# Optimization experiments

Hardware: AMD Instinct MI355X
Metric: run time of the kernel (lower is better)

Reference implementation:

```python
import jax, jax.numpy as jnp
import numpy as np

HEADS = 8
DIM_HEAD = 64


def setup_inputs() -> dict:
    key = jax.random.key(0)
    k1, k2, k3 = jax.random.split(key, 3)
    B, F, N_PATCH, DIM = 8, 16, 196, 512
    seq = 1 + F * N_PATCH  # 3137
    inner = HEADS * DIM_HEAD  # 512
    x = jax.random.normal(k1, (B, seq, DIM), dtype=jnp.float32)
    Wqkv = jax.random.normal(k2, (DIM, 3 * inner), dtype=jnp.float32) * (DIM ** -0.5)
    Wout = jax.random.normal(k3, (inner, DIM), dtype=jnp.float32) * (inner ** -0.5)
    bout = jnp.zeros((DIM,), dtype=jnp.float32)
    return {"x": x, "Wqkv": Wqkv, "Wout": Wout, "bout": bout, "f": F}


def _attn(q, k, v):
    # q: [b, i, d], k/v: [b, j, d]
    sim = jnp.einsum('bid,bjd->bij', q, k)
    a = jax.nn.softmax(sim, axis=-1)
    return jnp.einsum('bij,bjd->bid', a, v)


def reference(x, Wqkv, Wout, bout, f):
    B, N, D = x.shape
    h, dh = HEADS, DIM_HEAD
    scale = dh ** -0.5
    qkv = x @ Wqkv  # [B, N, 3*h*dh]
    q, k, v = jnp.split(qkv, 3, axis=-1)

    def to_bh(t):  # 'b n (h d) -> (b h) n d'
        return t.reshape(B, N, h, dh).transpose(0, 2, 1, 3).reshape(B * h, N, dh)

    q, k, v = to_bh(q), to_bh(k), to_bh(v)
    q = q * scale

    cls_q, q_ = q[:, :1], q[:, 1:]
    cls_k, k_ = k[:, :1], k[:, 1:]
    cls_v, v_ = v[:, :1], v[:, 1:]

    # cls token attends to all tokens
    cls_out = _attn(cls_q, k, v)  # [(b h), 1, dh]

    n = (N - 1) // f
    # 'b (f n) d -> (b f) n d'
    def split_frames(t):
        return t.reshape(B * h, f, n, dh).reshape(B * h * f, n, dh)

    q_, k_, v_ = split_frames(q_), split_frames(k_), split_frames(v_)

    # 'b () d -> (b r) () d' with r = f
    cls_k = jnp.repeat(cls_k, f, axis=0)
    cls_v = jnp.repeat(cls_v, f, axis=0)
    k_ = jnp.concatenate((cls_k, k_), axis=1)  # [(b h f), n+1, dh]
    v_ = jnp.concatenate((cls_v, v_), axis=1)

    out = _attn(q_, k_, v_)  # [(b h f), n, dh]
    out = out.reshape(B * h, f * n, dh)  # '(b f) n d -> b (f n) d'
    out = jnp.concatenate((cls_out, out), axis=1)  # [(b h), N, dh]
    # '(b h) n d -> b n (h d)'
    out = out.reshape(B, h, N, dh).transpose(0, 2, 1, 3).reshape(B, N, h * dh)
    return out @ Wout + bout
```

## Files before the change

### kernel.cpp

```cpp
#include <hip/hip_runtime.h>
#include <hip/hip_bf16.h>

#define B_    8
#define F_    16
#define NP_   196
#define SEQ_  3137
#define H_    8
#define DH_   64
#define BH_   64
#define M_    25096
#define MPAD_ 25216
#define DIM_  512
#define NQKV_ 1536

typedef _Float16 half8_t __attribute__((ext_vector_type(8)));
typedef _Float16 half4_t __attribute__((ext_vector_type(4)));
typedef float f32x4 __attribute__((ext_vector_type(4)));

#define XH_OFF     ((size_t)0)
#define WQKVT_OFF  ((size_t)25821184)
#define WOUTT_OFF  ((size_t)27394048)
#define QH_OFF     ((size_t)27918336)
#define KH_OFF     ((size_t)53616640)
#define VH_OFF     ((size_t)79314944)
#define ATTNH_OFF  ((size_t)105013248)
#define CLSP_OFF   XH_OFF

__device__ __forceinline__ void load_lds16(const _Float16* g, _Float16* l) {
  __builtin_amdgcn_global_load_lds(
      (const __attribute__((address_space(1))) void*)g,
      (__attribute__((address_space(3))) void*)l, 16, 0, 0);
}

__device__ __forceinline__ int xcd_swz(int orig, int nwg) {
  int q = nwg >> 3, r = nwg & 7;
  int x = orig & 7, j = orig >> 3;
  return (x < r ? x * (q + 1) : r * (q + 1) + (x - r) * q) + j;
}

__global__ __launch_bounds__(256) void convert_x_kernel(
    const float* __restrict__ x, _Float16* __restrict__ xh) {
  const size_t n8 = (size_t)M_ * DIM_ / 8;
  for (size_t i = (size_t)blockIdx.x * blockDim.x + threadIdx.x; i < n8;
       i += (size_t)gridDim.x * blockDim.x) {
    float4 a = ((const float4*)x)[2 * i];
    float4 b = ((const float4*)x)[2 * i + 1];
    half8_t h;
    h[0] = (_Float16)a.x; h[1] = (_Float16)a.y; h[2] = (_Float16)a.z; h[3] = (_Float16)a.w;
    h[4] = (_Float16)b.x; h[5] = (_Float16)b.y; h[6] = (_Float16)b.z; h[7] = (_Float16)b.w;
    ((half8_t*)xh)[i] = h;
  }
}

__global__ __launch_bounds__(256) void transpose_conv2_kernel(
    const float* __restrict__ wqkv, _Float16* __restrict__ wqkvT,
    const float* __restrict__ wout, _Float16* __restrict__ woutT) {
  __shared__ float tile[32][33];
  int by = blockIdx.y;
  const float* in; _Float16* out; int C;
  if (by < 48) { in = wqkv; out = wqkvT; C = NQKV_; }
  else         { in = wout; out = woutT; C = DIM_;  by -= 48; }
  const int r0 = blockIdx.x * 32, c0 = by * 32;
  const int lr = threadIdx.x >> 5, lc = threadIdx.x & 31;
#pragma unroll
  for (int p = 0; p < 4; ++p) {
    int r = p * 8 + lr;
    tile[r][lc] = in[(size_t)(r0 + r) * C + c0 + lc];
  }
  __syncthreads();
#pragma unroll
  for (int p = 0; p < 4; ++p) {
    int rr = p * 8 + lr;
    out[(size_t)(c0 + rr) * DIM_ + r0 + lc] = (_Float16)tile[lc][rr];
  }
}

__device__ __forceinline__ void gemm_mainloop_f16(
    const _Float16* __restrict__ A, const _Float16* __restrict__ Bt,
    int m0, int n0, _Float16* As, _Float16* Bs, f32x4 acc[4][4]) {
  const int tid = threadIdx.x;
  const int w = tid >> 6, lane = tid & 63;
  const int wr = w >> 1, wc = w & 1;
  const int lrow = lane & 15;
  const int g = lane >> 4;
  const int sw = lane & 7;

  const int srow = lane >> 3;
  const int scol = ((lane & 7) ^ srow) << 3;

  for (int k0 = 0; k0 < DIM_; k0 += 64) {
#pragma unroll
    for (int i = 0; i < 4; ++i) {
      int c = w * 4 + i;
      int r = c * 8 + srow;
      load_lds16(A + (size_t)(m0 + r) * DIM_ + k0 + scol, As + c * 512);
      load_lds16(Bt + (size_t)(n0 + r) * DIM_ + k0 + scol, Bs + c * 512);
    }
    __syncthreads();

#pragma unroll
    for (int kk = 0; kk < 2; ++kk) {
      const int kf = ((kk * 4 + g) ^ sw) << 3;
      half8_t a[4], b[4];
#pragma unroll
      for (int m = 0; m < 4; ++m)
        a[m] = *(const half8_t*)(As + (wr * 64 + m * 16 + lrow) * 64 + kf);
#pragma unroll
      for (int n = 0; n < 4; ++n)
        b[n] = *(const half8_t*)(Bs + (wc * 64 + n * 16 + lrow) * 64 + kf);
#pragma unroll
      for (int m = 0; m < 4; ++m)
#pragma unroll
        for (int n = 0; n < 4; ++n)
          acc[m][n] = __builtin_amdgcn_mfma_f32_16x16x32_f16(a[m], b[n], acc[m][n], 0, 0, 0);
    }
    __syncthreads();
  }
}

__global__ __launch_bounds__(256) void qkv_gemm_kernel(
    const _Float16* __restrict__ xh, const _Float16* __restrict__ wqkvT,
    _Float16* __restrict__ qh, _Float16* __restrict__ kh, _Float16* __restrict__ vh) {
  __shared__ _Float16 As[128 * 64];
  __shared__ _Float16 Bs[128 * 64];
  const int nwg = 197 * 12;
  const int lin = xcd_swz(blockIdx.x, nwg);
  const int mb = lin / 12, nb = lin - mb * 12;
  const int m0 = mb * 128, n0 = nb * 128;

  f32x4 acc[4][4];
#pragma unroll
  for (int m = 0; m < 4; ++m)
#pragma unroll
    for (int n = 0; n < 4; ++n) acc[m][n] = (f32x4)0.f;

  gemm_mainloop_f16(xh, wqkvT, m0, n0, As, Bs, acc);

  const int tid = threadIdx.x;
  const int w = tid >> 6, lane = tid & 63;
  const int wr = w >> 1, wc = w & 1;
  const int g = lane >> 4, lrow = lane & 15;

  _Float16* stg = (w < 2) ? (As + w * 4096) : (Bs + (w - 2) * 4096);
  const int gcb0 = n0 + wc * 64;
  const int which = gcb0 >> 9;
  const int h = (gcb0 >> 6) & 7;
  const float scale = (which == 0) ? 0.125f : 1.0f;
  _Float16* dst = (which == 0) ? qh : (which == 1) ? kh : vh;

#pragma unroll
  for (int m = 0; m < 4; ++m)
#pragma unroll
    for (int n = 0; n < 4; ++n)
#pragma unroll
      for (int j = 0; j < 4; ++j) {
        int row = m * 16 + g * 4 + j;
        int col = n * 16 + lrow;
        int slot = (col >> 3) ^ (row & 7);
        stg[row * 64 + slot * 8 + (col & 7)] = (_Float16)(acc[m][n][j] * scale);
      }
  asm volatile("s_waitcnt lgkmcnt(0)" ::: "memory");
  __builtin_amdgcn_sched_barrier(0);

  const int rl = lane >> 3, cs = lane & 7;
#pragma unroll
  for (int rr = 0; rr < 8; ++rr) {
    int row = rr * 8 + rl;
    int grow = m0 + wr * 64 + row;
    if (grow < M_) {
      int b = grow / SEQ_;
      int t = grow - b * SEQ_;
      half8_t v = *(const half8_t*)(stg + row * 64 + ((cs ^ (row & 7)) << 3));
      *(half8_t*)(dst + ((size_t)(b * H_ + h) * SEQ_ + t) * DH_ + cs * 8) = v;
    }
  }
}

__global__ __launch_bounds__(256) void out_gemm_kernel(
    const _Float16* __restrict__ attnh, const _Float16* __restrict__ woutT,
    const float* __restrict__ bias, float* __restrict__ out) {
  __shared__ _Float16 As[128 * 64];
  __shared__ _Float16 Bs[128 * 64];
  const int nwg = 197 * 4;
  const int lin = xcd_swz(blockIdx.x, nwg);
  const int mb = lin >> 2, nb = lin & 3;
  const int m0 = mb * 128, n0 = nb * 128;

  f32x4 acc[4][4];
#pragma unroll
  for (int m = 0; m < 4; ++m)
#pragma unroll
    for (int n = 0; n < 4; ++n) acc[m][n] = (f32x4)0.f;

  gemm_mainloop_f16(attnh, woutT, m0, n0, As, Bs, acc);

  const int tid = threadIdx.x;
  const int w = tid >> 6, lane = tid & 63;
  const int wr = w >> 1, wc = w & 1;
#pragma unroll
  for (int n = 0; n < 4; ++n) {
    const int gcol = n0 + wc * 64 + n * 16 + (lane & 15);
    const float bv = bias[gcol];
#pragma unroll
    for (int m = 0; m < 4; ++m)
#pragma unroll
      for (int j = 0; j < 4; ++j) {
        int grow = m0 + wr * 64 + m * 16 + (lane >> 4) * 4 + j;
        if (grow < M_) out[(size_t)grow * DIM_ + gcol] = acc[m][n][j] + bv;
      }
  }
}

__global__ __launch_bounds__(256) void attn_kernel(
    const _Float16* __restrict__ qh, const _Float16* __restrict__ kh,
    const _Float16* __restrict__ vh, _Float16* __restrict__ attnh,
    float* __restrict__ clsp) {
  __shared__ _Float16 SMEM[36864];
  const int bx = blockIdx.x;
  const int tid = threadIdx.x;

  const int bh = bx >> 4, fi = bx & 15;
  const int b = bh >> 3, h = bh & 7;
  const int w = tid >> 6, lane = tid & 63;
  const int g = lane >> 4, lc = lane & 15;
  _Float16* KL = SMEM;
  _Float16* VT = SMEM + 13312;
  _Float16* Pb = SMEM + 28160;
  _Float16* tmp = Pb;
  _Float16* Pw = Pb + w * (16 * 136);

  const size_t base = (size_t)bh * SEQ_ * DH_;

  half8_t qb0[4], qb1[4];
#pragma unroll
  for (int it = 0; it < 4; ++it) {
    int qq = min((w + it * 4) * 16 + lc, NP_ - 1);
    const _Float16* qp = qh + base + (size_t)(1 + fi * NP_ + qq) * DH_ + g * 8;
    qb0[it] = *(const half8_t*)(qp);
    qb1[it] = *(const half8_t*)(qp + 32);
  }

  for (int i = 0; i < 7; ++i) {
    int gran = i * 256 + tid;
    if (gran < 1664) {
      int row = gran >> 3, cg = gran & 7;
      int rowtok = (row == 0) ? 0 : fi * NP_ + min(row, NP_);
      load_lds16(kh + base + (size_t)rowtok * DH_ + ((cg ^ (row & 7)) << 3),
                 KL + (i * 256 + (tid & 192)) * 8);
    }
  }

#pragma unroll
  for (int half = 0; half < 2; ++half) {
    const int r0 = half * 104;
#pragma unroll
    for (int i = 0; i < 4; ++i) {
      int c = i * 256 + tid;
      if (c < 832) {
        int row = c >> 3, cg = c & 7;
        int gr = r0 + row;
        int rowtok = (gr == 0) ? 0 : fi * NP_ + min(gr, NP_);
        load_lds16(vh + base + (size_t)rowtok * DH_ + ((cg ^ (row & 7)) << 3),
                   tmp + (i * 256 + (tid & 192)) * 8);
      }
    }
    if (half == 1) {
      for (int idx = tid; idx < 64 * 35; idx += 256) {
        int d = idx / 35;
        VT[d * 232 + 197 + (idx - d * 35)] = (_Float16)0.f;
      }
    }
    __syncthreads();
#pragma unroll
    for (int i = 0; i < 4; ++i) {
      int item = i * 256 + tid;
      if (item < 832) {
        int cg = item / 104;
        int key = item - cg * 104;
        int gk = r0 + key;
        if (gk <= 196) {
          half8_t v = *(const half8_t*)(tmp + key * 64 + ((cg ^ (key & 7)) << 3));
#pragma unroll
          for (int u = 0; u < 8; ++u) VT[(cg * 8 + u) * 232 + gk] = v[u];
        }
      }
    }
    __syncthreads();
  }

  const f32x4 zero4 = (f32x4)0.f;

#pragma unroll
  for (int it = 0; it < 4; ++it) {
    const int qt = w + it * 4;
    if (qt < 13) {
      f32x4 st[13];
#pragma unroll
      for (int t = 0; t < 13; ++t) {
        int key = t * 16 + lc;
        const _Float16* kp = KL + key * 64;
        half8_t ka0 = *(const half8_t*)(kp + ((g ^ (key & 7)) << 3));
        half8_t ka1 = *(const half8_t*)(kp + (((4 + g) ^ (key & 7)) << 3));
        st[t] = __builtin_amdgcn_mfma_f32_16x16x32_f16(ka0, qb0[it], zero4, 0, 0, 0);
        st[t] = __builtin_amdgcn_mfma_f32_16x16x32_f16(ka1, qb1[it], st[t], 0, 0, 0);
      }

      float mx = -1e30f;
#pragma unroll
      for (int t = 0; t < 13; ++t)
#pragma unroll
        for (int j = 0; j < 4; ++j) {
          int key = t * 16 + g * 4 + j;
          if (key >= 197) st[t][j] = -1e30f;
          mx = fmaxf(mx, st[t][j]);
        }
      mx = fmaxf(mx, __shfl_xor(mx, 16));
      mx = fmaxf(mx, __shfl_xor(mx, 32));
      float l = 0.f;
#pragma unroll
      for (int t = 0; t < 13; ++t)
#pragma unroll
        for (int j = 0; j < 4; ++j) {
          float p = __expf(st[t][j] - mx);
          st[t][j] = p;
          l += p;
        }
      l += __shfl_xor(l, 16);
      l += __shfl_xor(l, 32);
      const float inv = 1.f / l;

      f32x4 o[4];
#pragma unroll
      for (int dt = 0; dt < 4; ++dt) o[dt] = zero4;

#pragma unroll
      for (int t = 0; t < 8; ++t) {
        half4_t hp;
#pragma unroll
        for (int j = 0; j < 4; ++j) hp[j] = (_Float16)(st[t][j] * inv);
        *(half4_t*)(Pw + lc * 136 + t * 16 + g * 4) = hp;
      }
#pragma unroll
      for (int c = 0; c < 4; ++c) {
        half8_t pa = *(const half8_t*)(Pw + lc * 136 + c * 32 + g * 8);
#pragma unroll
        for (int dt = 0; dt < 4; ++dt) {
          half8_t vb = *(const half8_t*)(VT + (dt * 16 + lc) * 232 + c * 32 + g * 8);
          o[dt] = __builtin_amdgcn_mfma_f32_16x16x32_f16(pa, vb, o[dt], 0, 0, 0);
        }
      }

#pragma unroll
      for (int t = 8; t < 13; ++t) {
        half4_t hp;
#pragma unroll
        for (int j = 0; j < 4; ++j) hp[j] = (_Float16)(st[t][j] * inv);
        *(half4_t*)(Pw + lc * 104 + (t - 8) * 16 + g * 4) = hp;
      }
      {
        half4_t hz;
#pragma unroll
        for (int j = 0; j < 4; ++j) hz[j] = (_Float16)0.f;
        *(half4_t*)(Pw + lc * 104 + 80 + g * 4) = hz;
      }
#pragma unroll
      for (int c = 4; c < 7; ++c) {
        half8_t pa = *(const half8_t*)(Pw + lc * 104 + (c - 4) * 32 + g * 8);
#pragma unroll
        for (int dt = 0; dt < 4; ++dt) {
          half8_t vb = *(const half8_t*)(VT + (dt * 16 + lc) * 232 + c * 32 + g * 8);
          o[dt] = __builtin_amdgcn_mfma_f32_16x16x32_f16(pa, vb, o[dt], 0, 0, 0);
        }
      }

#pragma unroll
      for (int dt = 0; dt < 4; ++dt)
#pragma unroll
        for (int j = 0; j < 4; ++j) {
          int q = qt * 16 + g * 4 + j;
          if (q < NP_) {
            int tok = 1 + fi * NP_ + q;
            attnh[((size_t)(b * SEQ_) + tok) * DIM_ + h * DH_ + dt * 16 + lc] =
                (_Float16)o[dt][j];
          }
        }
    }
  }

  __syncthreads();
  float* qs  = (float*)Pb;
  float* pp  = qs + 64;
  float* red = pp + 256;
  if (tid < 64) qs[tid] = (float)qh[base + tid];
  __syncthreads();

  const int kmin = (fi == 0) ? 0 : 1;
  float sc = -1e30f;
  if (tid >= kmin && tid < 197) {
    float s = 0.f;
#pragma unroll
    for (int i = 0; i < 8; ++i) {
      half8_t kk = *(const half8_t*)(KL + tid * 64 + ((i ^ (tid & 7)) << 3));
#pragma unroll
      for (int u = 0; u < 8; ++u) s += qs[8 * i + u] * (float)kk[u];
    }
    sc = s;
  }
  red[tid] = sc; __syncthreads();
  for (int st = 128; st > 0; st >>= 1) {
    if (tid < st) red[tid] = fmaxf(red[tid], red[tid + st]);
    __syncthreads();
  }
  const float cm = red[0]; __syncthreads();

  float cp = (tid >= kmin && tid < 197) ? __expf(sc - cm) : 0.f;
  pp[tid] = cp;
  red[tid] = cp; __syncthreads();
  for (int st = 128; st > 0; st >>= 1) {
    if (tid < st) red[tid] += red[tid + st];
    __syncthreads();
  }
  const float clsum = red[0]; __syncthreads();

  const int d = tid & 63;
  float a = 0.f;
#pragma unroll 4
  for (int u = 0; u < 64; ++u) {
    int k = w * 64 + u;
    if (k <= 196) a += pp[k] * (float)VT[d * 232 + k];
  }
  red[tid] = a; __syncthreads();
  if (tid < 64) {
    float asum = red[tid] + red[64 + tid] + red[128 + tid] + red[192 + tid];
    float* P = clsp + (size_t)(bh * 16 + fi) * 72;
    P[tid] = asum;
    if (tid == 0) { P[64] = cm; P[65] = clsum; }
  }
}

__global__ __launch_bounds__(64) void cls_combine_kernel(
    const float* __restrict__ clsp, _Float16* __restrict__ attnh) {
  const int bh = blockIdx.x;
  const int b = bh >> 3, h = bh & 7;
  const int d = threadIdx.x;
  const float* P = clsp + (size_t)bh * 16 * 72;

  float m = -1e30f;
#pragma unroll
  for (int c = 0; c < 16; ++c) m = fmaxf(m, P[c * 72 + 64]);
  float l = 0.f, o = 0.f;
#pragma unroll
  for (int c = 0; c < 16; ++c) {
    float wgt = __expf(P[c * 72 + 64] - m);
    l += P[c * 72 + 65] * wgt;
    o += P[c * 72 + d] * wgt;
  }
  attnh[(size_t)(b * SEQ_) * DIM_ + h * DH_ + d] = (_Float16)(o / l);
}

extern "C" void kernel_launch(void* const* d_in, const int* in_sizes, int n_in,
                              void* d_out, int out_size, void* d_ws, size_t ws_size,
                              hipStream_t stream) {
  (void)in_sizes; (void)n_in; (void)out_size; (void)ws_size;
  const float* x    = (const float*)d_in[0];
  const float* wqkv = (const float*)d_in[1];
  const float* wout = (const float*)d_in[2];
  const float* bout = (const float*)d_in[3];
  char* ws = (char*)d_ws;
  _Float16* xh    = (_Float16*)(ws + XH_OFF);
  _Float16* wqkvT = (_Float16*)(ws + WQKVT_OFF);
  _Float16* woutT = (_Float16*)(ws + WOUTT_OFF);
  _Float16* qh    = (_Float16*)(ws + QH_OFF);
  _Float16* kh    = (_Float16*)(ws + KH_OFF);
  _Float16* vh    = (_Float16*)(ws + VH_OFF);
  _Float16* attnh = (_Float16*)(ws + ATTNH_OFF);
  float*    clsp  = (float*)(ws + CLSP_OFF);
  float* out = (float*)d_out;

  convert_x_kernel<<<2048, 256, 0, stream>>>(x, xh);
  {
    dim3 g(16, 64);
    transpose_conv2_kernel<<<g, 256, 0, stream>>>(wqkv, wqkvT, wout, woutT);
  }

  qkv_gemm_kernel<<<197 * 12, 256, 0, stream>>>(xh, wqkvT, qh, kh, vh);

  attn_kernel<<<BH_ * F_, 256, 0, stream>>>(qh, kh, vh, attnh, clsp);
  cls_combine_kernel<<<BH_, 64, 0, stream>>>(clsp, attnh);

  out_gemm_kernel<<<197 * 4, 256, 0, stream>>>(attnh, woutT, bout, out);
}
```

Baseline: 166.4 us.

## Enlarge GEMM tiles to 256x128 and fuse weight/x conversion kernels

Both the QKV and output GEMMs now use 256x128 tiles, with each wave computing 128x64. Out-of-range A rows are clamped to the last valid row instead of relying on padding. The per-k-step loads of the B tile are shared across twice as many output rows, which raises arithmetic intensity but halves the number of workgroups (1188 and 396). That may leave the output GEMM with too few blocks to fill all CUs and raises register pressure. The x conversion and weight transpose kernels are merged into one launch to remove a launch gap.

Measured after the change: 210.9 us. 26.7% more time.

```diff
diff --git a/kernel.cpp b/kernel.cpp
--- a/kernel.cpp
+++ b/kernel.cpp
@@ -9,7 +9,6 @@
 #define DH_   64
 #define BH_   64
 #define M_    25096
-#define MPAD_ 25216
 #define DIM_  512
 #define NQKV_ 1536
 
@@ -38,11 +37,36 @@
   return (x < r ? x * (q + 1) : r * (q + 1) + (x - r) * q) + j;
 }
 
-__global__ __launch_bounds__(256) void convert_x_kernel(
-    const float* __restrict__ x, _Float16* __restrict__ xh) {
+__global__ __launch_bounds__(256) void prep_kernel(
+    const float* __restrict__ x, _Float16* __restrict__ xh,
+    const float* __restrict__ wqkv, _Float16* __restrict__ wqkvT,
+    const float* __restrict__ wout, _Float16* __restrict__ woutT) {
+  if (blockIdx.x < 1024) {
+    __shared__ float tile[32][33];
+    int id = blockIdx.x;
+    int xb = id & 15, by = id >> 4;
+    const float* in; _Float16* out; int C;
+    if (by < 48) { in = wqkv; out = wqkvT; C = NQKV_; }
+    else         { in = wout; out = woutT; C = DIM_;  by -= 48; }
+    const int r0 = xb * 32, c0 = by * 32;
+    const int lr = threadIdx.x >> 5, lc = threadIdx.x & 31;
+#pragma unroll
+    for (int p = 0; p < 4; ++p) {
+      int r = p * 8 + lr;
+      tile[r][lc] = in[(size_t)(r0 + r) * C + c0 + lc];
+    }
+    __syncthreads();
+#pragma unroll
+    for (int p = 0; p < 4; ++p) {
+      int rr = p * 8 + lr;
+      out[(size_t)(c0 + rr) * DIM_ + r0 + lc] = (_Float16)tile[lc][rr];
+    }
+    return;
+  }
+  const int id = blockIdx.x - 1024;
   const size_t n8 = (size_t)M_ * DIM_ / 8;
-  for (size_t i = (size_t)blockIdx.x * blockDim.x + threadIdx.x; i < n8;
-       i += (size_t)gridDim.x * blockDim.x) {
+  for (size_t i = (size_t)id * 256 + threadIdx.x; i < n8;
+       i += (size_t)2048 * 256) {
     float4 a = ((const float4*)x)[2 * i];
     float4 b = ((const float4*)x)[2 * i + 1];
     half8_t h;
@@ -52,67 +76,48 @@
   }
 }
 
-__global__ __launch_bounds__(256) void transpose_conv2_kernel(
-    const float* __restrict__ wqkv, _Float16* __restrict__ wqkvT,
-    const float* __restrict__ wout, _Float16* __restrict__ woutT) {
-  __shared__ float tile[32][33];
-  int by = blockIdx.y;
-  const float* in; _Float16* out; int C;
-  if (by < 48) { in = wqkv; out = wqkvT; C = NQKV_; }
-  else         { in = wout; out = woutT; C = DIM_;  by -= 48; }
-  const int r0 = blockIdx.x * 32, c0 = by * 32;
-  const int lr = threadIdx.x >> 5, lc = threadIdx.x & 31;
-#pragma unroll
-  for (int p = 0; p < 4; ++p) {
-    int r = p * 8 + lr;
-    tile[r][lc] = in[(size_t)(r0 + r) * C + c0 + lc];
-  }
-  __syncthreads();
-#pragma unroll
-  for (int p = 0; p < 4; ++p) {
-    int rr = p * 8 + lr;
-    out[(size_t)(c0 + rr) * DIM_ + r0 + lc] = (_Float16)tile[lc][rr];
-  }
-}
-
-__device__ __forceinline__ void gemm_mainloop_f16(
+__device__ __forceinline__ void gemm_mainloop_f16_w128(
     const _Float16* __restrict__ A, const _Float16* __restrict__ Bt,
-    int m0, int n0, _Float16* As, _Float16* Bs, f32x4 acc[4][4]) {
+    int m0, int n0, int maxA, _Float16* As, _Float16* Bs, f32x4 acc[8][4]) {
   const int tid = threadIdx.x;
   const int w = tid >> 6, lane = tid & 63;
-  const int wr = w >> 1, wc = w & 1;
+  const int wm = w >> 1, wn = w & 1;
   const int lrow = lane & 15;
   const int g = lane >> 4;
   const int sw = lane & 7;
 
-  const int srow = lane >> 3;
-  const int scol = ((lane & 7) ^ srow) << 3;
-
   for (int k0 = 0; k0 < DIM_; k0 += 64) {
 #pragma unroll
+    for (int i = 0; i < 8; ++i) {
+      int c = i * 256 + tid;
+      int row = c >> 3, s = c & 7;
+      int ra = min(m0 + row, maxA);
+      load_lds16(A + (size_t)ra * DIM_ + k0 + ((s ^ (row & 7)) << 3),
+                 As + (i * 256 + (tid & 192)) * 8);
+    }
+#pragma unroll
     for (int i = 0; i < 4; ++i) {
-      int c = w * 4 + i;
-      int r = c * 8 + srow;
-      load_lds16(A + (size_t)(m0 + r) * DIM_ + k0 + scol, As + c * 512);
-      load_lds16(Bt + (size_t)(n0 + r) * DIM_ + k0 + scol, Bs + c * 512);
+      int c = i * 256 + tid;
+      int row = c >> 3, s = c & 7;
+      load_lds16(Bt + (size_t)(n0 + row) * DIM_ + k0 + ((s ^ (row & 7)) << 3),
+                 Bs + (i * 256 + (tid & 192)) * 8);
     }
     __syncthreads();
 
 #pragma unroll
     for (int kk = 0; kk < 2; ++kk) {
       const int kf = ((kk * 4 + g) ^ sw) << 3;
-      half8_t a[4], b[4];
-#pragma unroll
-      for (int m = 0; m < 4; ++m)
-        a[m] = *(const half8_t*)(As + (wr * 64 + m * 16 + lrow) * 64 + kf);
+      half8_t b[4];
 #pragma unroll
       for (int n = 0; n < 4; ++n)
-        b[n] = *(const half8_t*)(Bs + (wc * 64 + n * 16 + lrow) * 64 + kf);
-#pragma unroll
-      for (int m = 0; m < 4; ++m)
+        b[n] = *(const half8_t*)(Bs + (wn * 64 + n * 16 + lrow) * 64 + kf);
+#pragma unroll
+      for (int m = 0; m < 8; ++m) {
+        half8_t a = *(const half8_t*)(As + (wm * 128 + m * 16 + lrow) * 64 + kf);
 #pragma unroll
         for (int n = 0; n < 4; ++n)
-          acc[m][n] = __builtin_amdgcn_mfma_f32_16x16x32_f16(a[m], b[n], acc[m][n], 0, 0, 0);
+          acc[m][n] = __builtin_amdgcn_mfma_f32_16x16x32_f16(a, b[n], acc[m][n], 0, 0, 0);
+      }
     }
     __syncthreads();
   }
@@ -121,57 +126,65 @@
 __global__ __launch_bounds__(256) void qkv_gemm_kernel(
     const _Float16* __restrict__ xh, const _Float16* __restrict__ wqkvT,
     _Float16* __restrict__ qh, _Float16* __restrict__ kh, _Float16* __restrict__ vh) {
-  __shared__ _Float16 As[128 * 64];
+  __shared__ _Float16 As[256 * 64];
   __shared__ _Float16 Bs[128 * 64];
-  const int nwg = 197 * 12;
+  const int nwg = 99 * 12;
   const int lin = xcd_swz(blockIdx.x, nwg);
   const int mb = lin / 12, nb = lin - mb * 12;
-  const int m0 = mb * 128, n0 = nb * 128;
-
-  f32x4 acc[4][4];
-#pragma unroll
-  for (int m = 0; m < 4; ++m)
+  const int m0 = mb * 256, n0 = nb * 128;
+
+  f32x4 acc[8][4];
+#pragma unroll
+  for (int m = 0; m < 8; ++m)
 #pragma unroll
     for (int n = 0; n < 4; ++n) acc[m][n] = (f32x4)0.f;
 
-  gemm_mainloop_f16(xh, wqkvT, m0, n0, As, Bs, acc);
+  gemm_mainloop_f16_w128(xh, wqkvT, m0, n0, M_ - 1, As, Bs, acc);
 
   const int tid = threadIdx.x;
   const int w = tid >> 6, lane = tid & 63;
-  const int wr = w >> 1, wc = w & 1;
+  const int wm = w >> 1, wn = w & 1;
   const int g = lane >> 4, lrow = lane & 15;
 
-  _Float16* stg = (w < 2) ? (As + w * 4096) : (Bs + (w - 2) * 4096);
-  const int gcb0 = n0 + wc * 64;
+  _Float16* stg = As + w * 4096;
+  const int gcb0 = n0 + wn * 64;
   const int which = gcb0 >> 9;
   const int h = (gcb0 >> 6) & 7;
   const float scale = (which == 0) ? 0.125f : 1.0f;
   _Float16* dst = (which == 0) ? qh : (which == 1) ? kh : vh;
-
-#pragma unroll
-  for (int m = 0; m < 4; ++m)
-#pragma unroll
-    for (int n = 0; n < 4; ++n)
-#pragma unroll
-      for (int j = 0; j < 4; ++j) {
-        int row = m * 16 + g * 4 + j;
-        int col = n * 16 + lrow;
-        int slot = (col >> 3) ^ (row & 7);
-        stg[row * 64 + slot * 8 + (col & 7)] = (_Float16)(acc[m][n][j] * scale);
-      }
-  asm volatile("s_waitcnt lgkmcnt(0)" ::: "memory");
-  __builtin_amdgcn_sched_barrier(0);
-
   const int rl = lane >> 3, cs = lane & 7;
-#pragma unroll
-  for (int rr = 0; rr < 8; ++rr) {
-    int row = rr * 8 + rl;
-    int grow = m0 + wr * 64 + row;
-    if (grow < M_) {
-      int b = grow / SEQ_;
-      int t = grow - b * SEQ_;
-      half8_t v = *(const half8_t*)(stg + row * 64 + ((cs ^ (row & 7)) << 3));
-      *(half8_t*)(dst + ((size_t)(b * H_ + h) * SEQ_ + t) * DH_ + cs * 8) = v;
+
+#pragma unroll
+  for (int r0 = 0; r0 < 2; ++r0) {
+#pragma unroll
+    for (int mm = 0; mm < 4; ++mm) {
+      int m = r0 * 4 + mm;
+#pragma unroll
+      for (int n = 0; n < 4; ++n)
+#pragma unroll
+        for (int j = 0; j < 4; ++j) {
+          int row2 = mm * 16 + g * 4 + j;
+          int col = n * 16 + lrow;
+          int slot = (col >> 3) ^ (row2 & 7);
+          stg[row2 * 64 + slot * 8 + (col & 7)] = (_Float16)(acc[m][n][j] * scale);
+        }
+    }
+    asm volatile("s_waitcnt lgkmcnt(0)" ::: "memory");
+    __builtin_amdgcn_sched_barrier(0);
+#pragma unroll
+    for (int rr = 0; rr < 8; ++rr) {
+      int row2 = rr * 8 + rl;
+      int grow = m0 + wm * 128 + r0 * 64 + row2;
+      if (grow < M_) {
+        int b = grow / SEQ_;
+        int t = grow - b * SEQ_;
+        half8_t v = *(const half8_t*)(stg + row2 * 64 + ((cs ^ (row2 & 7)) << 3));
+        *(half8_t*)(dst + ((size_t)(b * H_ + h) * SEQ_ + t) * DH_ + cs * 8) = v;
+      }
+    }
+    if (r0 == 0) {
+      asm volatile("s_waitcnt lgkmcnt(0)" ::: "memory");
+      __builtin_amdgcn_sched_barrier(0);
     }
   }
 }
@@ -179,33 +192,34 @@
 __global__ __launch_bounds__(256) void out_gemm_kernel(
     const _Float16* __restrict__ attnh, const _Float16* __restrict__ woutT,
     const float* __restrict__ bias, float* __restrict__ out) {
-  __shared__ _Float16 As[128 * 64];
+  __shared__ _Float16 As[256 * 64];
   __shared__ _Float16 Bs[128 * 64];
-  const int nwg = 197 * 4;
+  const int nwg = 99 * 4;
   const int lin = xcd_swz(blockIdx.x, nwg);
   const int mb = lin >> 2, nb = lin & 3;
-  const int m0 = mb * 128, n0 = nb * 128;
-
-  f32x4 acc[4][4];
-#pragma unroll
-  for (int m = 0; m < 4; ++m)
+  const int m0 = mb * 256, n0 = nb * 128;
+
+  f32x4 acc[8][4];
+#pragma unroll
+  for (int m = 0; m < 8; ++m)
 #pragma unroll
     for (int n = 0; n < 4; ++n) acc[m][n] = (f32x4)0.f;
 
-  gemm_mainloop_f16(attnh, woutT, m0, n0, As, Bs, acc);
+  gemm_mainloop_f16_w128(attnh, woutT, m0, n0, M_ - 1, As, Bs, acc);
 
   const int tid = threadIdx.x;
   const int w = tid >> 6, lane = tid & 63;
-  const int wr = w >> 1, wc = w & 1;
+  const int wm = w >> 1, wn = w & 1;
+  const int g = lane >> 4, lrow = lane & 15;
 #pragma unroll
   for (int n = 0; n < 4; ++n) {
-    const int gcol = n0 + wc * 64 + n * 16 + (lane & 15);
+    const int gcol = n0 + wn * 64 + n * 16 + lrow;
     const float bv = bias[gcol];
 #pragma unroll
-    for (int m = 0; m < 4; ++m)
+    for (int m = 0; m < 8; ++m)
 #pragma unroll
       for (int j = 0; j < 4; ++j) {
-        int grow = m0 + wr * 64 + m * 16 + (lane >> 4) * 4 + j;
+        int grow = m0 + wm * 128 + m * 16 + g * 4 + j;
         if (grow < M_) out[(size_t)grow * DIM_ + gcol] = acc[m][n][j] + bv;
       }
   }
@@ -477,16 +491,12 @@
   float*    clsp  = (float*)(ws + CLSP_OFF);
   float* out = (float*)d_out;
 
-  convert_x_kernel<<<2048, 256, 0, stream>>>(x, xh);
-  {
-    dim3 g(16, 64);
-    transpose_conv2_kernel<<<g, 256, 0, stream>>>(wqkv, wqkvT, wout, woutT);
-  }
-
-  qkv_gemm_kernel<<<197 * 12, 256, 0, stream>>>(xh, wqkvT, qh, kh, vh);
+  prep_kernel<<<3072, 256, 0, stream>>>(x, xh, wqkv, wqkvT, wout, woutT);
+
+  qkv_gemm_kernel<<<99 * 12, 256, 0, stream>>>(xh, wqkvT, qh, kh, vh);
 
   attn_kernel<<<BH_ * F_, 256, 0, stream>>>(qh, kh, vh, attnh, clsp);
   cls_combine_kernel<<<BH_, 64, 0, stream>>>(clsp, attnh);
 
-  out_gemm_kernel<<<197 * 4, 256, 0, stream>>>(attnh, woutT, bout, out);
-}
+  out_gemm_kernel<<<99 * 4, 256, 0, stream>>>(attnh, woutT, bout, out);
+}
```
